# Kernel optimization log

Hardware: AMD Instinct MI355X
Metric: run time of the kernel (lower is better)

Reference implementation:

```python
import jax, jax.numpy as jnp
import numpy as np

# Neuron / sim params from init_kwargs
THETA = 1.0        # thr
TAU_RHO = 0.5      # grad_width (surrogate width, used only in backward)
SCALE_RHO = 1.0    # grad_scale
NUM_TS = 100


def avg_pool4(x):
    # SLAYER pool(4): conv3d with constant weight 1/16 over 4x4 spatial, stride 4 == average pool
    N, C, H, W, T = x.shape
    return x.reshape(N, C, H // 4, 4, W // 4, 4, T).mean(axis=(3, 5))


def conv7(x, w):
    # torch Conv3d over (H, W, T) with kernel (7,7,1), padding (3,3,0), stride 1, no bias
    return jax.lax.conv_general_dilated(
        x, w, window_strides=(1, 1, 1),
        padding=((3, 3), (3, 3), (0, 0)),
        dimension_numbers=('NCHWT', 'OIHWT', 'NCHWT'))


def psp(x):
    # IAF synaptic kernel = Heaviside step => psp is cumulative sum over time (Ts = 1)
    return jnp.cumsum(x, axis=-1)


def spike_scan(p):
    # Integrate-and-fire spike generation with reset-by-subtraction (scaleRef=1):
    # v[t] = psp[t] - theta * (#spikes before t); spike when v[t] >= theta.
    p_t = jnp.moveaxis(p, -1, 0)  # [T, N, C, H, W]
    count0 = jnp.zeros(p.shape[:-1], p.dtype)

    def step(count, pt):
        v = pt - THETA * count
        s = (v >= THETA).astype(pt.dtype)
        return count + s, (s, v)

    _, (s, v) = jax.lax.scan(step, count0, p_t)
    return jnp.moveaxis(s, 0, -1), jnp.moveaxis(v, 0, -1)


def setup_inputs() -> dict:
    key = jax.random.key(0)
    k0, k1, k2, k3 = jax.random.split(key, 4)
    data = jax.random.uniform(k0, (8, 2, 256, 256, NUM_TS), dtype=jnp.float32)
    # learned parameters (bias=False in SLAYER conv/dense)
    w_conv0 = jax.random.normal(k1, (4, 2, 7, 7, 1), dtype=jnp.float32) * 0.2
    w_conv1 = jax.random.normal(k2, (8, 4, 7, 7, 1), dtype=jnp.float32) * 0.2
    w_dense = jax.random.normal(k3, (2, 8, 4, 4, 1), dtype=jnp.float32) * 0.2
    return {"data": data, "w_conv0": w_conv0, "w_conv1": w_conv1, "w_dense": w_dense}


def reference(data, w_conv0, w_conv1, w_dense):
    x = conv7(avg_pool4(data), w_conv0)     # [8,4,64,64,T]
    s0, _ = spike_scan(psp(x))
    x = conv7(avg_pool4(s0), w_conv1)       # [8,8,16,16,T]
    s1, _ = spike_scan(psp(x))
    x = avg_pool4(s1)                       # [8,8,4,4,T]
    # dense((4,4,8) -> 2): conv3d whose kernel spans the full spatial extent
    out = jnp.einsum('nchwt,ochw->not', x, w_dense[..., 0])  # [8,2,T]
    return out
```

## Files before the change

kernel.cpp:

```cpp
#include <hip/hip_runtime.h>
#include <hip/hip_bf16.h>
#include <stdint.h>


#define T_ 100

__global__ __launch_bounds__(256) void k1_pool0(const float* __restrict__ in,
                                                double* __restrict__ out) {
    __shared__ double lds[64 * 101];
    int b = blockIdx.x;
    int h = b & 63, c = (b >> 6) & 1, n = b >> 7;
    const float* inb = in + ((size_t)((n * 2 + c) * 256 + 4 * h) * 256) * 100;
    for (int k = 0; k < 7; ++k) {
        int e = threadIdx.x + (k << 8);
        if (e < 1600) {
            int w = e / 25, tq = e % 25;
            double s0 = 0.0, s1 = 0.0, s2 = 0.0, s3 = 0.0;
            #pragma unroll
            for (int a = 0; a < 4; ++a) {
                #pragma unroll
                for (int bb = 0; bb < 4; ++bb) {
                    const float4 v = *reinterpret_cast<const float4*>(
                        &inb[((size_t)(a * 256 + 4 * w + bb)) * 100 + 4 * tq]);
                    s0 += (double)v.x;
                    s1 += (double)v.y;
                    s2 += (double)v.z;
                    s3 += (double)v.w;
                }
            }
            double* lp = &lds[w * 101 + 4 * tq];
            lp[0] = s0 * 0.0625;
            lp[1] = s1 * 0.0625;
            lp[2] = s2 * 0.0625;
            lp[3] = s3 * 0.0625;
        }
    }
    __syncthreads();
    double* outb = out + ((size_t)(n * 2 + c) * 100) * 4096 + h * 64;
    for (int k = 0; k < 25; ++k) {
        int oi = threadIdx.x + (k << 8);
        int t = oi >> 6, w = oi & 63;
        outb[(size_t)t * 4096 + w] = lds[w * 101 + t];
    }
}

__global__ __launch_bounds__(256) void k2a_conv0(const double* __restrict__ pooled0,
                                                 const float* __restrict__ wc0,
                                                 double* __restrict__ x0) {
    __shared__ double tile[2 * 22 * 70];
    __shared__ double wlds[392];
    int b = blockIdx.x;
    int hs = b & 3;
    int t = (b >> 2) % 100;
    int n = b / 400;
    int tid = threadIdx.x;

    for (int i = tid; i < 392; i += 256) wlds[i] = (double)wc0[i];
    for (int k = 0; k < 13; ++k) {
        int e = tid + (k << 8);
        if (e < 3080) {
            int ci = e / 1540, rem = e % 1540;
            int row = rem / 70, ww = rem % 70;
            int habs = hs * 16 + row - 3;
            int wabs = ww - 3;
            double v = 0.0;
            if ((unsigned)habs < 64u && (unsigned)wabs < 64u)
                v = pooled0[((size_t)((n * 2 + ci) * 100 + t)) * 4096 + habs * 64 + wabs];
            tile[(ci * 22 + row) * 70 + ww] = v;
        }
    }
    __syncthreads();

    int w = tid & 63, hq = tid >> 6;
    int hl0 = hq * 4;
    double acc[4][4];
    #pragma unroll
    for (int co = 0; co < 4; ++co)
        #pragma unroll
        for (int j = 0; j < 4; ++j) acc[co][j] = 0.0;

    for (int ci = 0; ci < 2; ++ci) {
        for (int kh = 0; kh < 7; ++kh) {
            const double* r0 = &tile[(ci * 22 + hl0 + kh) * 70 + w];
            const double* wp = &wlds[ci * 49 + kh * 7];
            #pragma unroll
            for (int kw = 0; kw < 7; ++kw) {
                double v0 = r0[kw];
                double v1 = r0[70 + kw];
                double v2 = r0[140 + kw];
                double v3 = r0[210 + kw];
                #pragma unroll
                for (int co = 0; co < 4; ++co) {
                    double wv = wp[co * 98 + kw];
                    acc[co][0] += v0 * wv;
                    acc[co][1] += v1 * wv;
                    acc[co][2] += v2 * wv;
                    acc[co][3] += v3 * wv;
                }
            }
        }
    }
    #pragma unroll
    for (int co = 0; co < 4; ++co)
        #pragma unroll
        for (int j = 0; j < 4; ++j)
            x0[((size_t)((n * 4 + co) * 100 + t)) * 4096 + (hs * 16 + hl0 + j) * 64 + w] =
                acc[co][j];
}

__global__ __launch_bounds__(256) void k2b_scan0(const double* __restrict__ x0,
                                                 uint8_t* __restrict__ s0) {
    int bid = blockIdx.x;
    size_t base = (size_t)(bid >> 4) * (100 * 4096) + ((bid & 15) << 8) + threadIdx.x;
    double p = 0.0;
    int cnt = 0;
    for (int tc = 0; tc < 10; ++tc) {
        double v[10];
        #pragma unroll
        for (int j = 0; j < 10; ++j)
            v[j] = x0[base + (size_t)(tc * 10 + j) * 4096];
        #pragma unroll
        for (int j = 0; j < 10; ++j) {
            p += v[j];
            int sp = (p - (double)cnt) >= 1.0;
            cnt += sp;
            s0[base + (size_t)(tc * 10 + j) * 4096] = (uint8_t)sp;
        }
    }
}

#define TC2 5
__global__ __launch_bounds__(128) void k2_conv0_scan(const double* __restrict__ pooled0,
                                                     const float* __restrict__ wc0,
                                                     uint8_t* __restrict__ s0) {
    __shared__ double tile[2 * 7 * TC2 * 70];
    int b = blockIdx.x;
    int h = b & 63, n = b >> 6;
    int tid = threadIdx.x;
    int w = tid & 63, cog = tid >> 6;
    int co0 = 2 * cog, co1 = co0 + 1;
    for (int i = tid; i < 2 * 7 * TC2 * 70; i += 128) tile[i] = 0.0;
    double p0 = 0.0, p1 = 0.0;
    int c0 = 0, c1 = 0;
    for (int ch = 0; ch < T_ / TC2; ++ch) {
        int t0 = ch * TC2;
        __syncthreads();
        for (int k = 0; k < 35; ++k) {
            int e = tid + (k << 7);
            int ww = e & 63, rowid = e >> 6;
            int ci = rowid / 35, rem = rowid % 35;
            int tt = rem / 7, r = rem % 7;
            int habs = h - 3 + r;
            if ((unsigned)habs < 64u)
                tile[((ci * 7 + r) * TC2 + tt) * 70 + ww + 3] =
                    pooled0[((size_t)((n * 2 + ci) * 100 + t0 + tt)) * 4096 + habs * 64 + ww];
        }
        __syncthreads();
        double acc0[TC2], acc1[TC2];
        #pragma unroll
        for (int tt = 0; tt < TC2; ++tt) { acc0[tt] = 0.0; acc1[tt] = 0.0; }
        for (int ci = 0; ci < 2; ++ci) {
            for (int kh = 0; kh < 7; ++kh) {
                const double* trow = &tile[((ci * 7 + kh) * TC2) * 70];
                const float* wr0 = &wc0[co0 * 98 + ci * 49 + kh * 7];
                const float* wr1 = &wc0[co1 * 98 + ci * 49 + kh * 7];
                #pragma unroll
                for (int kw = 0; kw < 7; ++kw) {
                    double wa = (double)wr0[kw];
                    double wb = (double)wr1[kw];
                    #pragma unroll
                    for (int tt = 0; tt < TC2; ++tt) {
                        double v = trow[tt * 70 + w + kw];
                        acc0[tt] += v * wa;
                        acc1[tt] += v * wb;
                    }
                }
            }
        }
        #pragma unroll
        for (int tt = 0; tt < TC2; ++tt) {
            size_t ob = ((size_t)((n * 4 + co0) * 100 + t0 + tt)) * 4096 + h * 64 + w;
            p0 += acc0[tt];
            int sp0 = (p0 - (double)c0) >= 1.0;
            c0 += sp0;
            s0[ob] = (uint8_t)sp0;
            size_t ob1 = ((size_t)((n * 4 + co1) * 100 + t0 + tt)) * 4096 + h * 64 + w;
            p1 += acc1[tt];
            int sp1 = (p1 - (double)c1) >= 1.0;
            c1 += sp1;
            s0[ob1] = (uint8_t)sp1;
        }
    }
}

__global__ __launch_bounds__(256) void k3_pool1(const uint8_t* __restrict__ s0,
                                                float* __restrict__ pooled1) {
    int oi = blockIdx.x * 256 + threadIdx.x;
    int w = oi & 15, h = (oi >> 4) & 15;
    int tc = oi >> 8;
    int t = tc % 100, nc = tc / 100;
    const uint8_t* base = s0 + ((size_t)nc * 100 + t) * 4096;
    int isum = 0;
    #pragma unroll
    for (int a = 0; a < 4; ++a) {
        uint32_t v = *reinterpret_cast<const uint32_t*>(&base[(4 * h + a) * 64 + 4 * w]);
        isum += (int)(v & 0xffu) + (int)((v >> 8) & 0xffu) +
                (int)((v >> 16) & 0xffu) + (int)(v >> 24);
    }
    pooled1[oi] = (float)isum * 0.0625f;
}

__global__ __launch_bounds__(256) void k4a_conv1(const float* __restrict__ pooled1,
                                                 const float* __restrict__ wc1,
                                                 double* __restrict__ x1) {
    __shared__ float tile[4 * 22 * 24];
    int b = blockIdx.x;
    int n = b / 100, t = b % 100;
    int tid = threadIdx.x;
    for (int i = tid; i < 4 * 22 * 24; i += 256) tile[i] = 0.0f;
    __syncthreads();
    for (int k = 0; k < 4; ++k) {
        int e = tid + (k << 8);
        int w = e & 15, rowid = e >> 4;
        int ci = rowid >> 4, hr3 = rowid & 15;
        tile[(ci * 22 + hr3 + 3) * 24 + 3 + w] =
            pooled1[((size_t)((n * 4 + ci) * 100 + t)) * 256 + hr3 * 16 + w];
    }
    __syncthreads();
    int h = tid >> 4, w = tid & 15;
    double acc[8];
    #pragma unroll
    for (int co = 0; co < 8; ++co) acc[co] = 0.0;
    for (int ci = 0; ci < 4; ++ci) {
        for (int kh = 0; kh < 7; ++kh) {
            const float* trow = &tile[(ci * 22 + h + kh) * 24];
            const float* wr = &wc1[ci * 49 + kh * 7];
            #pragma unroll
            for (int kw = 0; kw < 7; ++kw) {
                double v = (double)trow[w + kw];
                #pragma unroll
                for (int co = 0; co < 8; ++co)
                    acc[co] += v * (double)wr[co * 196 + kw];
            }
        }
    }
    #pragma unroll
    for (int co = 0; co < 8; ++co)
        x1[((size_t)((n * 8 + co) * 100 + t)) * 256 + tid] = acc[co];
}

__global__ __launch_bounds__(256) void k4b_scan1(const double* __restrict__ x1,
                                                 uint8_t* __restrict__ s1) {
    size_t base = (size_t)blockIdx.x * 100 * 256 + threadIdx.x;
    double p = 0.0;
    int cnt = 0;
    for (int tc = 0; tc < 10; ++tc) {
        double v[10];
        #pragma unroll
        for (int j = 0; j < 10; ++j)
            v[j] = x1[base + (size_t)(tc * 10 + j) * 256];
        #pragma unroll
        for (int j = 0; j < 10; ++j) {
            p += v[j];
            int sp = (p - (double)cnt) >= 1.0;
            cnt += sp;
            s1[base + (size_t)(tc * 10 + j) * 256] = (uint8_t)sp;
        }
    }
}

__global__ __launch_bounds__(256) void k5_dense(const uint8_t* __restrict__ s1,
                                                const float* __restrict__ wd,
                                                float* __restrict__ out) {
    __shared__ float red[2][4];
    int b = blockIdx.x;
    int n = b / 100, t = b % 100;
    int tid = threadIdx.x;
    int c = tid >> 5, H = (tid >> 1) & 15, Wg = tid & 1;
    const uint8_t* sb = s1 + ((size_t)((n * 8 + c) * 100 + t)) * 256 + H * 16 + Wg * 8;
    float sumA = 0.f, sumB = 0.f;
    #pragma unroll
    for (int j = 0; j < 4; ++j) sumA += (float)sb[j];
    #pragma unroll
    for (int j = 4; j < 8; ++j) sumB += (float)sb[j];
    int wb = c * 16 + (H >> 2) * 4 + Wg * 2;
    float o0 = sumA * wd[wb] + sumB * wd[wb + 1];
    float o1 = sumA * wd[128 + wb] + sumB * wd[128 + wb + 1];
    #pragma unroll
    for (int off = 32; off > 0; off >>= 1) {
        o0 += __shfl_down(o0, off, 64);
        o1 += __shfl_down(o1, off, 64);
    }
    int lane = tid & 63, wid = tid >> 6;
    if (lane == 0) { red[0][wid] = o0; red[1][wid] = o1; }
    __syncthreads();
    if (tid == 0) {
        float a = (red[0][0] + red[0][1]) + (red[0][2] + red[0][3]);
        float bsum = (red[1][0] + red[1][1]) + (red[1][2] + red[1][3]);
        out[(size_t)(n * 2) * 100 + t] = a * 0.0625f;
        out[(size_t)(n * 2 + 1) * 100 + t] = bsum * 0.0625f;
    }
}

extern "C" void kernel_launch(void* const* d_in, const int* in_sizes, int n_in,
                              void* d_out, int out_size, void* d_ws, size_t ws_size,
                              hipStream_t stream) {
    const float* data = (const float*)d_in[0];
    const float* w0   = (const float*)d_in[1];
    const float* w1   = (const float*)d_in[2];
    const float* wd   = (const float*)d_in[3];
    float* out = (float*)d_out;
    char* ws = (char*)d_ws;

    const size_t NEED_SPLIT = 157286400;

    if (ws_size >= NEED_SPLIT) {
        double*  pooled0 = (double*)(ws);
        double*  x0      = (double*)(ws + 52428800);
        uint8_t* s0      = (uint8_t*)(ws);
        float*   pooled1 = (float*)(ws + 13107200);
        double*  x1      = (double*)(ws + 16384000);
        uint8_t* s1      = (uint8_t*)(ws + 32768000);

        k1_pool0<<<1024, 256, 0, stream>>>(data, pooled0);
        k2a_conv0<<<3200, 256, 0, stream>>>(pooled0, w0, x0);
        k2b_scan0<<<512, 256, 0, stream>>>(x0, s0);
        k3_pool1<<<3200, 256, 0, stream>>>(s0, pooled1);
        k4a_conv1<<<800, 256, 0, stream>>>(pooled1, w1, x1);
        k4b_scan1<<<64, 256, 0, stream>>>(x1, s1);
        k5_dense<<<800, 256, 0, stream>>>(s1, wd, out);
    } else {
        double*  pooled0 = (double*)(ws);
        double*  x1      = (double*)(ws + 52428800);
        uint8_t* s0      = (uint8_t*)(ws + 68812800);
        float*   pooled1 = (float*)(ws + 81920000);
        uint8_t* s1      = (uint8_t*)(ws + 85196800);

        k1_pool0<<<1024, 256, 0, stream>>>(data, pooled0);
        k2_conv0_scan<<<512, 128, 0, stream>>>(pooled0, w0, s0);
        k3_pool1<<<3200, 256, 0, stream>>>(s0, pooled1);
        k4a_conv1<<<800, 256, 0, stream>>>(pooled1, w1, x1);
        k4b_scan1<<<64, 256, 0, stream>>>(x1, s1);
        k5_dense<<<800, 256, 0, stream>>>(s1, wd, out);
    }
}
```

Measured before the change: 244.3 us.

## Fuse layer-0 spike scan with 4x4 pooling and streamline conv tile loads

The layer-0 spike scan kernel now keeps each 10-timestep chunk of spikes in shared memory and writes the 4x4-pooled result directly. This removes the separate pool kernel and the global round trip of the uint8 spike tensor. The conv0 tile load is restructured so each wavefront loads one padded row, avoiding per-element division and modulo. Conv1 weights are staged in shared memory instead of being read from global memory in the inner loop. The fused scan adds two block barriers per chunk, and workspace offsets are rearranged.

```diff
diff --git a/kernel.cpp b/kernel.cpp
--- a/kernel.cpp
+++ b/kernel.cpp
@@ -56,17 +56,22 @@
     int tid = threadIdx.x;
 
     for (int i = tid; i < 392; i += 256) wlds[i] = (double)wc0[i];
-    for (int k = 0; k < 13; ++k) {
-        int e = tid + (k << 8);
-        if (e < 3080) {
-            int ci = e / 1540, rem = e % 1540;
-            int row = rem / 70, ww = rem % 70;
+    {
+        int lane = tid & 63, wv = tid >> 6;
+        for (int r = wv; r < 44; r += 4) {
+            int ci = (r >= 22) ? 1 : 0;
+            int row = r - ci * 22;
             int habs = hs * 16 + row - 3;
-            int wabs = ww - 3;
-            double v = 0.0;
-            if ((unsigned)habs < 64u && (unsigned)wabs < 64u)
-                v = pooled0[((size_t)((n * 2 + ci) * 100 + t)) * 4096 + habs * 64 + wabs];
-            tile[(ci * 22 + row) * 70 + ww] = v;
+            const double* src =
+                &pooled0[((size_t)((n * 2 + ci) * 100 + t)) * 4096 + habs * 64];
+            double* dst = &tile[(ci * 22 + row) * 70];
+            int wabs = lane - 3;
+            bool hok = (unsigned)habs < 64u;
+            dst[lane] = (hok && (unsigned)wabs < 64u) ? src[wabs] : 0.0;
+            if (lane < 6) {
+                int wabs2 = lane + 61;
+                dst[lane + 64] = (hok && (unsigned)wabs2 < 64u) ? src[wabs2] : 0.0;
+            }
         }
     }
     __syncthreads();
@@ -108,10 +113,13 @@
                 acc[co][j];
 }
 
-__global__ __launch_bounds__(256) void k2b_scan0(const double* __restrict__ x0,
-                                                 uint8_t* __restrict__ s0) {
+__global__ __launch_bounds__(256) void k2b_scan0_pool(const double* __restrict__ x0,
+                                                      float* __restrict__ pooled1) {
+    __shared__ uint8_t lsp[10][256];
     int bid = blockIdx.x;
-    size_t base = (size_t)(bid >> 4) * (100 * 4096) + ((bid & 15) << 8) + threadIdx.x;
+    int g = bid >> 4, rg = bid & 15;
+    int tid = threadIdx.x;
+    size_t base = (size_t)g * (100 * 4096) + ((size_t)rg << 8) + tid;
     double p = 0.0;
     int cnt = 0;
     for (int tc = 0; tc < 10; ++tc) {
@@ -124,8 +132,22 @@
             p += v[j];
             int sp = (p - (double)cnt) >= 1.0;
             cnt += sp;
-            s0[base + (size_t)(tc * 10 + j) * 4096] = (uint8_t)sp;
-        }
+            lsp[j][tid] = (uint8_t)sp;
+        }
+        __syncthreads();
+        if (tid < 160) {
+            int t = tid >> 4, wp = tid & 15;
+            int isum = 0;
+            #pragma unroll
+            for (int r = 0; r < 4; ++r) {
+                uint32_t u = *reinterpret_cast<const uint32_t*>(&lsp[t][r * 64 + 4 * wp]);
+                isum += (int)(u & 0xffu) + (int)((u >> 8) & 0xffu) +
+                        (int)((u >> 16) & 0xffu) + (int)(u >> 24);
+            }
+            pooled1[((size_t)g * 100 + tc * 10 + t) * 256 + rg * 16 + wp] =
+                (float)isum * 0.0625f;
+        }
+        __syncthreads();
     }
 }
 
@@ -214,10 +236,12 @@
                                                  const float* __restrict__ wc1,
                                                  double* __restrict__ x1) {
     __shared__ float tile[4 * 22 * 24];
+    __shared__ float wl[1568];
     int b = blockIdx.x;
     int n = b / 100, t = b % 100;
     int tid = threadIdx.x;
     for (int i = tid; i < 4 * 22 * 24; i += 256) tile[i] = 0.0f;
+    for (int i = tid; i < 1568; i += 256) wl[i] = wc1[i];
     __syncthreads();
     for (int k = 0; k < 4; ++k) {
         int e = tid + (k << 8);
@@ -234,7 +258,7 @@
     for (int ci = 0; ci < 4; ++ci) {
         for (int kh = 0; kh < 7; ++kh) {
             const float* trow = &tile[(ci * 22 + h + kh) * 24];
-            const float* wr = &wc1[ci * 49 + kh * 7];
+            const float* wr = &wl[ci * 49 + kh * 7];
             #pragma unroll
             for (int kw = 0; kw < 7; ++kw) {
                 double v = (double)trow[w + kw];
@@ -317,23 +341,21 @@
     if (ws_size >= NEED_SPLIT) {
         double*  pooled0 = (double*)(ws);
         double*  x0      = (double*)(ws + 52428800);
-        uint8_t* s0      = (uint8_t*)(ws);
-        float*   pooled1 = (float*)(ws + 13107200);
-        double*  x1      = (double*)(ws + 16384000);
-        uint8_t* s1      = (uint8_t*)(ws + 32768000);
+        float*   pooled1 = (float*)(ws);
+        double*  x1      = (double*)(ws + 4194304);
+        uint8_t* s1      = (uint8_t*)(ws + 25165824);
 
         k1_pool0<<<1024, 256, 0, stream>>>(data, pooled0);
         k2a_conv0<<<3200, 256, 0, stream>>>(pooled0, w0, x0);
-        k2b_scan0<<<512, 256, 0, stream>>>(x0, s0);
-        k3_pool1<<<3200, 256, 0, stream>>>(s0, pooled1);
+        k2b_scan0_pool<<<512, 256, 0, stream>>>(x0, pooled1);
         k4a_conv1<<<800, 256, 0, stream>>>(pooled1, w1, x1);
         k4b_scan1<<<64, 256, 0, stream>>>(x1, s1);
         k5_dense<<<800, 256, 0, stream>>>(s1, wd, out);
     } else {
         double*  pooled0 = (double*)(ws);
-        double*  x1      = (double*)(ws + 52428800);
-        uint8_t* s0      = (uint8_t*)(ws + 68812800);
-        float*   pooled1 = (float*)(ws + 81920000);
+        uint8_t* s0      = (uint8_t*)(ws + 52428800);
+        float*   pooled1 = (float*)(ws + 65536000);
+        double*  x1      = (double*)(ws + 68812800);
         uint8_t* s1      = (uint8_t*)(ws + 85196800);
 
         k1_pool0<<<1024, 256, 0, stream>>>(data, pooled0);
```

Result: slower. 250.2 us (+2.4%).
